# Kernel tuning notes

Measured on AMD Instinct MI355X. Metric: run time of the kernel, lower is better.

## Reference

```python
import jax, jax.numpy as jnp
import numpy as np

B, L, D, H, S = 16, 512, 512, 16, 3
FF = 4 * D
DH = D // H
EPS = 1e-5


def _bn(x, g, b):
    # BatchNorm1d in training mode: x is (B, C, L); biased variance over (B, L).
    m = jnp.mean(x, axis=(0, 2), keepdims=True)
    v = jnp.var(x, axis=(0, 2), keepdims=True)
    return (x - m) * jax.lax.rsqrt(v + EPS) * g[None, :, None] + b[None, :, None]


def setup_inputs() -> dict:
    key = jax.random.key(0)
    ks = jax.random.split(key, 8)
    s = 0.05
    return {
        "x": jax.random.normal(ks[0], (B, L, D), jnp.float32),
        "emb": jax.random.normal(ks[1], (D, D), jnp.float32) * s,  # emb[0], (in, out); hidden==input_dim
        "bn2_g": jnp.ones((D,), jnp.float32),
        "bn2_b": jnp.zeros((D,), jnp.float32),
        "Wq": jax.random.normal(ks[2], (S, D, D), jnp.float32) * s,  # stored (in,out)
        "bq": jnp.zeros((S, D), jnp.float32),
        "Wk": jax.random.normal(ks[3], (S, D, D), jnp.float32) * s,
        "bk": jnp.zeros((S, D), jnp.float32),
        "Wv": jax.random.normal(ks[4], (S, D, D), jnp.float32) * s,
        "bv": jnp.zeros((S, D), jnp.float32),
        "bna_g": jnp.ones((S, D), jnp.float32),
        "bna_b": jnp.zeros((S, D), jnp.float32),
        "W1": jax.random.normal(ks[5], (S, D, FF), jnp.float32) * s,  # conv1 1x1, (in,out)
        "b1": jnp.zeros((S, FF), jnp.float32),
        "W2": jax.random.normal(ks[6], (S, FF, D), jnp.float32) * s,  # conv2 1x1, (in,out)
        "b2": jnp.zeros((S, D), jnp.float32),
        "bnf_g": jnp.ones((S, D), jnp.float32),
        "bnf_b": jnp.zeros((S, D), jnp.float32),
    }


def _split_heads(t):
    # torch.cat(torch.split(t, D//H, dim=2), dim=0): (B,L,D) -> (H*B, L, DH), head-major on dim0.
    return jnp.moveaxis(t.reshape(B, L, H, DH), 2, 0).reshape(H * B, L, DH)


def reference(x, emb, bn2_g, bn2_b, Wq, bq, Wk, bk, Wv, bv, bna_g, bna_b,
              W1, b1, W2, b2, bnf_g, bnf_b):
    scale = 1.0 / np.sqrt(DH).astype(np.float32)
    xp = jnp.swapaxes(x, 1, 2)                      # (B, D, L)
    enc = jnp.einsum('bil,io->bol', xp, emb)        # 1x1 conv embedding, no bias
    enc = _bn(enc, bn2_g, bn2_b)                    # (B, D, L)
    for i in range(S):
        xin = jnp.swapaxes(enc, 1, 2)               # (B, L, D)
        Q = jax.nn.relu(xin @ Wq[i] + bq[i])
        K = jax.nn.relu(xin @ Wk[i] + bk[i])
        V = jax.nn.relu(xin @ Wv[i] + bv[i])
        Q_, K_, V_ = _split_heads(Q), _split_heads(K), _split_heads(V)  # (H*B, L, DH)
        sc = jnp.einsum('nqd,nkd->nqk', Q_, K_) * scale                 # (H*B, L, L)
        att = jax.nn.softmax(sc, axis=0)            # softmax over batch*heads dim (as in source)
        o = jnp.einsum('nqk,nkd->nqd', att, V_)     # (H*B, L, DH)
        # torch.cat(torch.split(o, B, dim=0), dim=2): (H*B,L,DH) -> (B,L,D)
        o = o.reshape(H, B, L, DH).transpose(1, 2, 0, 3).reshape(B, L, D)
        o = o + xin
        enc = _bn(jnp.swapaxes(o, 1, 2), bna_g[i], bna_b[i])            # (B, D, L)
        # FeedForward: 1x1 conv -> relu -> 1x1 conv -> residual -> BN
        h1 = jax.nn.relu(jnp.einsum('bdl,df->bfl', enc, W1[i]) + b1[i][None, :, None])
        h2 = jnp.einsum('bfl,fd->bdl', h1, W2[i]) + b2[i][None, :, None]
        enc = _bn(h2 + enc, bnf_g[i], bnf_b[i])
    return jnp.swapaxes(enc, 1, 2)                  # (B, L, D)
```

## Files before the change

### kernel.cpp

```cpp
#include <hip/hip_runtime.h>

#define DEVI __device__ __forceinline__

typedef unsigned short u16;
typedef __attribute__((ext_vector_type(8))) short s16x8;
typedef __attribute__((ext_vector_type(4))) float f32x4;
typedef __attribute__((ext_vector_type(4))) unsigned short u16x4v;
typedef __attribute__((ext_vector_type(2))) unsigned int u32x2;

constexpr int NB   = 16;
constexpr int LL   = 512;
constexpr int DD   = 512;
constexpr int FF_  = 2048;
constexpr int NROW = NB * LL;
constexpr float C2 = 0.17677669529663687f * 1.4426950408889634f;
constexpr size_t QKVOFF = (size_t)NROW * DD;

DEVI u16 f2b(float f) {
  unsigned int u = __float_as_uint(f);
  unsigned int r = u + 0x7FFFu + ((u >> 16) & 1u);
  return (u16)(r >> 16);
}

DEVI void gload16(const void* g, void* l) {
  __builtin_amdgcn_global_load_lds(
      (const __attribute__((address_space(1))) unsigned int*)(unsigned long long)g,
      (__attribute__((address_space(3))) unsigned int*)(unsigned int)(unsigned long long)l,
      16, 0, 0);
}

__global__ __launch_bounds__(256) void k_f32_to_bf16(const float* __restrict__ X, u16* __restrict__ Y, int n4) {
  for (int i = blockIdx.x * 256 + threadIdx.x; i < n4; i += gridDim.x * 256) {
    float4 x = ((const float4*)X)[i];
    u16x4v o; o[0] = f2b(x.x); o[1] = f2b(x.y); o[2] = f2b(x.z); o[3] = f2b(x.w);
    ((u16x4v*)Y)[i] = o;
  }
}

__global__ __launch_bounds__(256) void k_zero(float* __restrict__ p, int n) {
  int i = blockIdx.x * 256 + threadIdx.x;
  if (i < n) p[i] = 0.f;
}

__global__ __launch_bounds__(256) void k_recip(float* __restrict__ p, int n) {
  int i = blockIdx.x * 256 + threadIdx.x;
  if (i < n) p[i] = 1.0f / p[i];
}

__global__ void k_catbias(const float* __restrict__ a, const float* __restrict__ b,
                          const float* __restrict__ c, float* __restrict__ o) {
  int i = blockIdx.x * 256 + threadIdx.x;
  o[i] = (i < 512) ? a[i] : (i < 1024) ? b[i - 512] : c[i - 1024];
}

__global__ __launch_bounds__(256) void k_wtrans(const float* __restrict__ W, u16* __restrict__ WT, int K, int M) {
  __shared__ float tile[32][33];
  const int k0 = blockIdx.x * 32, m0 = blockIdx.y * 32;
  const int tx = threadIdx.x & 31, ty = threadIdx.x >> 5;
#pragma unroll
  for (int j = 0; j < 4; ++j) tile[ty + j * 8][tx] = W[(size_t)(k0 + ty + j * 8) * M + m0 + tx];
  __syncthreads();
#pragma unroll
  for (int j = 0; j < 4; ++j) WT[(size_t)(m0 + ty + j * 8) * K + k0 + tx] = f2b(tile[tx][ty + j * 8]);
}

template <int BM, int RELU, int HASB, int HASRES, int OUTF, int OUTB, int SPLIT3>
__global__ __launch_bounds__(256) void k_gemm(const u16* __restrict__ A, const u16* __restrict__ Bt,
                                              const float* __restrict__ bias, const float* __restrict__ Res,
                                              float* __restrict__ Cf, u16* __restrict__ Cb,
                                              int K, int Ncols) {
  constexpr int WR = BM / 64;
  constexpr int WC = 4 / WR;
  constexpr int MW = 4;
  constexpr int NW = 128 / (16 * WC);
  __shared__ __align__(16) u16 As[BM * 64];
  __shared__ __align__(16) u16 Bs[128 * 64];
  const int t = threadIdx.x, lane = t & 63, w = t >> 6;
  const int wr = w / WC, wc = w % WC, l16 = lane & 15, lhi = lane >> 4;
  const int row0 = blockIdx.x * BM, col0 = blockIdx.y * 128;
  const int sr = lane >> 3, sc = (lane & 7) * 8;
  const u16* Ag = A + (size_t)(row0 + sr) * K + sc;
  const u16* Bg = Bt + (size_t)(col0 + sr) * K + sc;

  f32x4 acc[MW][NW] = {};

  for (int k0 = 0; k0 < K; k0 += 64) {
    __syncthreads();
#pragma unroll
    for (int j = 0; j < BM / 32; ++j) {
      const int ch = w * (BM / 32) + j;
      gload16(Ag + (size_t)(ch * 8) * K + k0, As + ch * 512);
    }
#pragma unroll
    for (int j = 0; j < 4; ++j) {
      const int ch = w * 4 + j;
      gload16(Bg + (size_t)(ch * 8) * K + k0, Bs + ch * 512);
    }
    __syncthreads();
#pragma unroll
    for (int kk = 0; kk < 2; ++kk) {
      s16x8 af[MW], bfv[NW];
#pragma unroll
      for (int m = 0; m < MW; ++m) af[m] = *(const s16x8*)(As + (wr * 64 + m * 16 + l16) * 64 + kk * 32 + lhi * 8);
#pragma unroll
      for (int n = 0; n < NW; ++n) bfv[n] = *(const s16x8*)(Bs + (wc * (16 * NW) + n * 16 + l16) * 64 + kk * 32 + lhi * 8);
#pragma unroll
      for (int m = 0; m < MW; ++m)
#pragma unroll
        for (int n = 0; n < NW; ++n)
          acc[m][n] = __builtin_amdgcn_mfma_f32_16x16x32_bf16(af[m], bfv[n], acc[m][n], 0, 0, 0);
    }
  }

#pragma unroll
  for (int n = 0; n < NW; ++n) {
    const int col = col0 + wc * (16 * NW) + n * 16 + l16;
    float bv = 0.f;
    if constexpr (HASB) bv = bias[col];
#pragma unroll
    for (int m = 0; m < MW; ++m) {
      const int rbase = row0 + wr * 64 + m * 16 + lhi * 4;
#pragma unroll
      for (int r = 0; r < 4; ++r) {
        float v = acc[m][n][r] + bv;
        if constexpr (RELU) v = fmaxf(v, 0.f);
        const int row = rbase + r;
        const size_t idx = (size_t)row * Ncols + col;
        if constexpr (HASRES) v += Res[idx];
        if constexpr (OUTF) Cf[idx] = v;
        if constexpr (OUTB) {
          if constexpr (SPLIT3) {
            const size_t ib = (size_t)(col >> 9) * QKVOFF + (size_t)row * DD + (col & 511);
            Cb[ib] = f2b(v);
          } else {
            Cb[idx] = f2b(v);
          }
        }
      }
    }
  }
}

__global__ __launch_bounds__(256) void k_attn_z(const u16* __restrict__ Q, const u16* __restrict__ Kt,
                                                float* __restrict__ Z) {
  const int t = threadIdx.x, lane = t & 63, w = t >> 6;
  const int l16 = lane & 15, lhi = lane >> 4;
  const int q0 = blockIdx.x * 64 + (w >> 1) * 32;
  const int k0 = blockIdx.y * 64 + (w & 1) * 32;
  const int n0 = blockIdx.z * 16;
  f32x4 zac[2][2] = {};
  for (int nn = 0; nn < 16; ++nn) {
    const int n = n0 + nn, h = n >> 4, b = n & 15;
    const size_t base = (size_t)b * LL * DD + (size_t)h * 32;
    s16x8 a[2], bb[2];
#pragma unroll
    for (int mi = 0; mi < 2; ++mi) a[mi] = *(const s16x8*)(Q + base + (size_t)(q0 + mi * 16 + l16) * DD + lhi * 8);
#pragma unroll
    for (int ni = 0; ni < 2; ++ni) bb[ni] = *(const s16x8*)(Kt + base + (size_t)(k0 + ni * 16 + l16) * DD + lhi * 8);
#pragma unroll
    for (int mi = 0; mi < 2; ++mi)
#pragma unroll
      for (int ni = 0; ni < 2; ++ni) {
        f32x4 z4 = {0.f, 0.f, 0.f, 0.f};
        f32x4 s = __builtin_amdgcn_mfma_f32_16x16x32_bf16(a[mi], bb[ni], z4, 0, 0, 0);
#pragma unroll
        for (int r = 0; r < 4; ++r) zac[mi][ni][r] += exp2f(s[r] * C2);
      }
  }
#pragma unroll
  for (int mi = 0; mi < 2; ++mi)
#pragma unroll
    for (int ni = 0; ni < 2; ++ni)
#pragma unroll
      for (int r = 0; r < 4; ++r)
        atomicAdd(&Z[(q0 + mi * 16 + lhi * 4 + r) * LL + k0 + ni * 16 + l16], zac[mi][ni][r]);
}

__global__ __launch_bounds__(512) void k_attn_pv3(const u16* __restrict__ Q, const u16* __restrict__ K,
                                                  const u16* __restrict__ V, const float* __restrict__ IZ,
                                                  const float* __restrict__ Res, float* __restrict__ T) {
  __shared__ __align__(16) u16 Kl[512 * 40];
  __shared__ __align__(16) u16 Vl[32 * 520];
  __shared__ __align__(16) u16 Pl[8][1024];
  const int n = blockIdx.x, h = n >> 4, b = n & 15;
  const int t = threadIdx.x, lane = t & 63, w = t >> 6;
  const int l16 = lane & 15, lhi = lane >> 4;
  const size_t base = (size_t)b * LL * DD + (size_t)h * 32;

#pragma unroll
  for (int j = 0; j < 4; ++j) {
    const int c = t + j * 512;
    const int k = c >> 2, part = c & 3;
    const s16x8 v = *(const s16x8*)(K + base + (size_t)k * DD + part * 8);
    *(s16x8*)(Kl + k * 40 + part * 8) = v;
  }
#pragma unroll
  for (int j = 0; j < 4; ++j) {
    const int c = t + j * 512;
    const int k = c >> 2, dp = c & 3;
    const s16x8 v = *(const s16x8*)(V + base + (size_t)k * DD + dp * 8);
#pragma unroll
    for (int jj = 0; jj < 8; ++jj) Vl[(dp * 8 + jj) * 520 + k] = (u16)v[jj];
  }
  const int qbase = w * 64;
  s16x8 aqv[4];
#pragma unroll
  for (int qf = 0; qf < 4; ++qf)
    aqv[qf] = *(const s16x8*)(Q + base + (size_t)(qbase + qf * 16 + l16) * DD + lhi * 8);
  __syncthreads();

  char* P = (char*)&Pl[w][0];
  const int wxor = (l16 & 7) << 4;
  const int wbase = l16 * 128 + lhi * 8;

#pragma unroll
  for (int qf = 0; qf < 4; ++qf) {
    const int q16 = qbase + qf * 16;
    const float* izrow = IZ + (size_t)(q16 + l16) * LL + lhi * 4;
    f32x4 oa[2] = {};
#pragma unroll
    for (int kt = 0; kt < 8; ++kt) {
      const int kb = kt * 64;
      f32x4 s[4]; float4 iz[4];
#pragma unroll
      for (int ks = 0; ks < 4; ++ks) {
        const s16x8 af = *(const s16x8*)(Kl + (kb + ks * 16 + l16) * 40 + lhi * 8);
        f32x4 z4 = {0.f, 0.f, 0.f, 0.f};
        s[ks] = __builtin_amdgcn_mfma_f32_16x16x32_bf16(af, aqv[qf], z4, 0, 0, 0);
        iz[ks] = *(const float4*)(izrow + kb + ks * 16);
      }
#pragma unroll
      for (int ks = 0; ks < 4; ++ks) {
        const float p0 = exp2f(s[ks][0] * C2) * iz[ks].x;
        const float p1 = exp2f(s[ks][1] * C2) * iz[ks].y;
        const float p2 = exp2f(s[ks][2] * C2) * iz[ks].z;
        const float p3 = exp2f(s[ks][3] * C2) * iz[ks].w;
        unsigned int pk0, pk1;
        asm("v_cvt_pk_bf16_f32 %0, %1, %2" : "=v"(pk0) : "v"(p0), "v"(p1));
        asm("v_cvt_pk_bf16_f32 %0, %1, %2" : "=v"(pk1) : "v"(p2), "v"(p3));
        u32x2 pw; pw[0] = pk0; pw[1] = pk1;
        *(u32x2*)(P + ((wbase + ks * 32) ^ wxor)) = pw;
      }
#pragma unroll
      for (int kc = 0; kc < 2; ++kc) {
        const s16x8 pa = *(const s16x8*)(P + ((l16 * 128 + kc * 64 + lhi * 16) ^ wxor));
#pragma unroll
        for (int dt = 0; dt < 2; ++dt) {
          const s16x8 bv = *(const s16x8*)(Vl + (dt * 16 + l16) * 520 + kb + kc * 32 + lhi * 8);
          oa[dt] = __builtin_amdgcn_mfma_f32_16x16x32_bf16(pa, bv, oa[dt], 0, 0, 0);
        }
      }
    }
#pragma unroll
    for (int dt = 0; dt < 2; ++dt)
#pragma unroll
      for (int r = 0; r < 4; ++r) {
        const size_t idx = (size_t)(b * LL + q16 + lhi * 4 + r) * DD + h * 32 + dt * 16 + l16;
        T[idx] = oa[dt][r] + Res[idx];
      }
  }
}

__global__ __launch_bounds__(256) void k_bn_stats(const float* __restrict__ X, float* __restrict__ S) {
  const int t = threadIdx.x;
  const int r0 = blockIdx.x * 32;
  float s0 = 0.f, q0 = 0.f, s1 = 0.f, q1 = 0.f;
  for (int r = 0; r < 32; ++r) {
    const float x0 = X[(size_t)(r0 + r) * DD + t];
    const float x1 = X[(size_t)(r0 + r) * DD + t + 256];
    s0 += x0; q0 += x0 * x0; s1 += x1; q1 += x1 * x1;
  }
  atomicAdd(&S[t], s0);
  atomicAdd(&S[t + 256], s1);
  atomicAdd(&S[512 + t], q0);
  atomicAdd(&S[512 + t + 256], q1);
}

__global__ void k_bn_fin(float* __restrict__ S, const float* __restrict__ g,
                         const float* __restrict__ be, float* __restrict__ coef) {
  const int d = threadIdx.x;
  const float inv = 1.0f / 8192.0f;
  const float mean = S[d] * inv;
  const float var = S[512 + d] * inv - mean * mean;
  const float a = rsqrtf(var + 1e-5f) * g[d];
  coef[d] = a;
  coef[512 + d] = be[d] - mean * a;
  S[d] = 0.f; S[512 + d] = 0.f;
}

template <int WB>
__global__ __launch_bounds__(256) void k_bn_apply(const float* __restrict__ X, const float* __restrict__ coef,
                                                  float* __restrict__ Yf, u16* __restrict__ Yb) {
  const int n4 = NROW * DD / 4;
  for (int i = blockIdx.x * 256 + threadIdx.x; i < n4; i += gridDim.x * 256) {
    const float4 xv = ((const float4*)X)[i];
    const int d = (i & 127) * 4;
    const float y0 = fmaf(xv.x, coef[d + 0], coef[512 + d + 0]);
    const float y1 = fmaf(xv.y, coef[d + 1], coef[512 + d + 1]);
    const float y2 = fmaf(xv.z, coef[d + 2], coef[512 + d + 2]);
    const float y3 = fmaf(xv.w, coef[d + 3], coef[512 + d + 3]);
    ((float4*)Yf)[i] = make_float4(y0, y1, y2, y3);
    if constexpr (WB) {
      u16x4v o; o[0] = f2b(y0); o[1] = f2b(y1); o[2] = f2b(y2); o[3] = f2b(y3);
      ((u16x4v*)Yb)[i] = o;
    }
  }
}

extern "C" void kernel_launch(void* const* d_in, const int* in_sizes, int n_in,
                              void* d_out, int out_size, void* d_ws, size_t ws_size,
                              hipStream_t stream) {
  const float* x    = (const float*)d_in[0];
  const float* emb  = (const float*)d_in[1];
  const float* bn2g = (const float*)d_in[2];
  const float* bn2b = (const float*)d_in[3];
  const float* Wq   = (const float*)d_in[4];
  const float* bq   = (const float*)d_in[5];
  const float* Wk   = (const float*)d_in[6];
  const float* bkp  = (const float*)d_in[7];
  const float* Wv   = (const float*)d_in[8];
  const float* bvp  = (const float*)d_in[9];
  const float* bnag = (const float*)d_in[10];
  const float* bnab = (const float*)d_in[11];
  const float* W1   = (const float*)d_in[12];
  const float* b1   = (const float*)d_in[13];
  const float* W2   = (const float*)d_in[14];
  const float* b2   = (const float*)d_in[15];
  const float* bnfg = (const float*)d_in[16];
  const float* bnfb = (const float*)d_in[17];

  char* p = (char*)d_ws;
  auto alloc = [&](size_t bytes) { char* r = p; p += (bytes + 255) & ~(size_t)255; return r; };
  u16*   xb    = (u16*)alloc((size_t)NROW * DD * 2);
  float* encF  = (float*)alloc((size_t)NROW * DD * 4);
  u16*   encB  = (u16*)alloc((size_t)NROW * DD * 2);
  float* tF    = (float*)alloc((size_t)NROW * DD * 4);
  u16*   qkv   = (u16*)alloc((size_t)3 * NROW * DD * 2);
  u16*   h1    = (u16*)alloc((size_t)NROW * FF_ * 2);
  float* Z     = (float*)alloc((size_t)LL * LL * 4);
  float* sums  = (float*)alloc(1024 * 4);
  float* coef  = (float*)alloc(1024 * 4);
  float* bqkv  = (float*)alloc(1536 * 4);
  u16*   embT  = (u16*)alloc((size_t)DD * DD * 2);
  u16*   wqkvT = (u16*)alloc((size_t)3 * DD * DD * 2);
  u16*   w1T   = (u16*)alloc((size_t)DD * FF_ * 2);
  u16*   w2T   = (u16*)alloc((size_t)FF_ * DD * 2);
  if ((size_t)(p - (char*)d_ws) > ws_size) return;

  auto run_bn = [&](const float* Xs, const float* g, const float* be, float* Yf, u16* Yb) {
    k_bn_stats<<<256, 256, 0, stream>>>(Xs, sums);
    k_bn_fin<<<1, 512, 0, stream>>>(sums, g, be, coef);
    if (Yb) k_bn_apply<1><<<2048, 256, 0, stream>>>(Xs, coef, Yf, Yb);
    else    k_bn_apply<0><<<2048, 256, 0, stream>>>(Xs, coef, Yf, nullptr);
  };

  k_zero<<<4, 256, 0, stream>>>(sums, 1024);
  k_f32_to_bf16<<<2048, 256, 0, stream>>>(x, xb, NROW * DD / 4);
  k_wtrans<<<dim3(16, 16), 256, 0, stream>>>(emb, embT, DD, DD);
  k_gemm<64, 0, 0, 0, 1, 0, 0><<<dim3(128, 4), 256, 0, stream>>>(xb, embT, nullptr, nullptr, tF, nullptr, DD, DD);
  run_bn(tF, bn2g, bn2b, encF, encB);

  for (int i = 0; i < 3; ++i) {
    k_wtrans<<<dim3(16, 16), 256, 0, stream>>>(Wq + (size_t)i * DD * DD, wqkvT, DD, DD);
    k_wtrans<<<dim3(16, 16), 256, 0, stream>>>(Wk + (size_t)i * DD * DD, wqkvT + (size_t)512 * DD, DD, DD);
    k_wtrans<<<dim3(16, 16), 256, 0, stream>>>(Wv + (size_t)i * DD * DD, wqkvT + (size_t)1024 * DD, DD, DD);
    k_catbias<<<6, 256, 0, stream>>>(bq + i * DD, bkp + i * DD, bvp + i * DD, bqkv);
    k_gemm<128, 1, 1, 0, 0, 1, 1><<<dim3(64, 12), 256, 0, stream>>>(encB, wqkvT, bqkv, nullptr, nullptr, qkv, DD, 1536);
    k_zero<<<1024, 256, 0, stream>>>(Z, LL * LL);
    k_attn_z<<<dim3(8, 8, 16), 256, 0, stream>>>(qkv, qkv + QKVOFF, Z);
    k_recip<<<1024, 256, 0, stream>>>(Z, LL * LL);
    k_attn_pv3<<<256, 512, 0, stream>>>(qkv, qkv + QKVOFF, qkv + 2 * QKVOFF, Z, encF, tF);
    run_bn(tF, bnag + i * DD, bnab + i * DD, encF, encB);
    k_wtrans<<<dim3(16, 64), 256, 0, stream>>>(W1 + (size_t)i * DD * FF_, w1T, DD, FF_);
    k_gemm<128, 1, 1, 0, 0, 1, 0><<<dim3(64, 16), 256, 0, stream>>>(encB, w1T, b1 + i * FF_, nullptr, nullptr, h1, DD, FF_);
    k_wtrans<<<dim3(64, 16), 256, 0, stream>>>(W2 + (size_t)i * FF_ * DD, w2T, FF_, DD);
    k_gemm<64, 0, 1, 1, 1, 0, 0><<<dim3(128, 4), 256, 0, stream>>>(h1, w2T, b2 + i * DD, encF, tF, nullptr, FF_, DD);
    float* yf = (i == 2) ? (float*)d_out : encF;
    run_bn(tF, bnfg + i * DD, bnfb + i * DD, yf, (i == 2) ? nullptr : encB);
  }
}
```

Baseline: 728.6 us.

## Fuse BatchNorm statistics into GEMM and attention epilogues

```diff
diff --git a/kernel.cpp b/kernel.cpp
--- a/kernel.cpp
+++ b/kernel.cpp
@@ -64,11 +64,11 @@
   for (int j = 0; j < 4; ++j) WT[(size_t)(m0 + ty + j * 8) * K + k0 + tx] = f2b(tile[tx][ty + j * 8]);
 }
 
-template <int BM, int RELU, int HASB, int HASRES, int OUTF, int OUTB, int SPLIT3>
+template <int BM, int RELU, int HASB, int HASRES, int OUTF, int OUTB, int STATS, int SPLIT3>
 __global__ __launch_bounds__(256) void k_gemm(const u16* __restrict__ A, const u16* __restrict__ Bt,
                                               const float* __restrict__ bias, const float* __restrict__ Res,
                                               float* __restrict__ Cf, u16* __restrict__ Cb,
-                                              int K, int Ncols) {
+                                              float* __restrict__ stats, int K, int Ncols) {
   constexpr int WR = BM / 64;
   constexpr int WC = 4 / WR;
   constexpr int MW = 4;
@@ -117,6 +117,7 @@
     const int col = col0 + wc * (16 * NW) + n * 16 + l16;
     float bv = 0.f;
     if constexpr (HASB) bv = bias[col];
+    float ssum = 0.f, ssq = 0.f;
 #pragma unroll
     for (int m = 0; m < MW; ++m) {
       const int rbase = row0 + wr * 64 + m * 16 + lhi * 4;
@@ -136,6 +137,15 @@
             Cb[idx] = f2b(v);
           }
         }
+        if constexpr (STATS) { ssum += v; ssq += v * v; }
+      }
+    }
+    if constexpr (STATS) {
+      ssum += __shfl_xor(ssum, 16); ssq += __shfl_xor(ssq, 16);
+      ssum += __shfl_xor(ssum, 32); ssq += __shfl_xor(ssq, 32);
+      if (lhi == 0) {
+        atomicAdd(&stats[col], ssum);
+        atomicAdd(&stats[512 + col], ssq);
       }
     }
   }
@@ -178,7 +188,8 @@
 
 __global__ __launch_bounds__(512) void k_attn_pv3(const u16* __restrict__ Q, const u16* __restrict__ K,
                                                   const u16* __restrict__ V, const float* __restrict__ IZ,
-                                                  const float* __restrict__ Res, float* __restrict__ T) {
+                                                  const float* __restrict__ Res, float* __restrict__ T,
+                                                  float* __restrict__ stats) {
   __shared__ __align__(16) u16 Kl[512 * 40];
   __shared__ __align__(16) u16 Vl[32 * 520];
   __shared__ __align__(16) u16 Pl[8][1024];
@@ -212,6 +223,7 @@
   char* P = (char*)&Pl[w][0];
   const int wxor = (l16 & 7) << 4;
   const int wbase = l16 * 128 + lhi * 8;
+  float ssum[2] = {0.f, 0.f}, ssq[2] = {0.f, 0.f};
 
 #pragma unroll
   for (int qf = 0; qf < 4; ++qf) {
@@ -256,24 +268,22 @@
 #pragma unroll
       for (int r = 0; r < 4; ++r) {
         const size_t idx = (size_t)(b * LL + q16 + lhi * 4 + r) * DD + h * 32 + dt * 16 + l16;
-        T[idx] = oa[dt][r] + Res[idx];
-      }
-  }
-}
-
-__global__ __launch_bounds__(256) void k_bn_stats(const float* __restrict__ X, float* __restrict__ S) {
-  const int t = threadIdx.x;
-  const int r0 = blockIdx.x * 32;
-  float s0 = 0.f, q0 = 0.f, s1 = 0.f, q1 = 0.f;
-  for (int r = 0; r < 32; ++r) {
-    const float x0 = X[(size_t)(r0 + r) * DD + t];
-    const float x1 = X[(size_t)(r0 + r) * DD + t + 256];
-    s0 += x0; q0 += x0 * x0; s1 += x1; q1 += x1 * x1;
-  }
-  atomicAdd(&S[t], s0);
-  atomicAdd(&S[t + 256], s1);
-  atomicAdd(&S[512 + t], q0);
-  atomicAdd(&S[512 + t + 256], q1);
+        const float v = oa[dt][r] + Res[idx];
+        T[idx] = v;
+        ssum[dt] += v; ssq[dt] += v * v;
+      }
+  }
+#pragma unroll
+  for (int dt = 0; dt < 2; ++dt) {
+    float su = ssum[dt], sq = ssq[dt];
+    su += __shfl_xor(su, 16); sq += __shfl_xor(sq, 16);
+    su += __shfl_xor(su, 32); sq += __shfl_xor(sq, 32);
+    if (lhi == 0) {
+      const int col = h * 32 + dt * 16 + l16;
+      atomicAdd(&stats[col], su);
+      atomicAdd(&stats[512 + col], sq);
+    }
+  }
 }
 
 __global__ void k_bn_fin(float* __restrict__ S, const float* __restrict__ g,
@@ -348,7 +358,6 @@
   if ((size_t)(p - (char*)d_ws) > ws_size) return;
 
   auto run_bn = [&](const float* Xs, const float* g, const float* be, float* Yf, u16* Yb) {
-    k_bn_stats<<<256, 256, 0, stream>>>(Xs, sums);
     k_bn_fin<<<1, 512, 0, stream>>>(sums, g, be, coef);
     if (Yb) k_bn_apply<1><<<2048, 256, 0, stream>>>(Xs, coef, Yf, Yb);
     else    k_bn_apply<0><<<2048, 256, 0, stream>>>(Xs, coef, Yf, nullptr);
@@ -357,7 +366,7 @@
   k_zero<<<4, 256, 0, stream>>>(sums, 1024);
   k_f32_to_bf16<<<2048, 256, 0, stream>>>(x, xb, NROW * DD / 4);
   k_wtrans<<<dim3(16, 16), 256, 0, stream>>>(emb, embT, DD, DD);
-  k_gemm<64, 0, 0, 0, 1, 0, 0><<<dim3(128, 4), 256, 0, stream>>>(xb, embT, nullptr, nullptr, tF, nullptr, DD, DD);
+  k_gemm<128, 0, 0, 0, 1, 0, 1, 0><<<dim3(64, 4), 256, 0, stream>>>(xb, embT, nullptr, nullptr, tF, nullptr, sums, DD, DD);
   run_bn(tF, bn2g, bn2b, encF, encB);
 
   for (int i = 0; i < 3; ++i) {
@@ -365,16 +374,16 @@
     k_wtrans<<<dim3(16, 16), 256, 0, stream>>>(Wk + (size_t)i * DD * DD, wqkvT + (size_t)512 * DD, DD, DD);
     k_wtrans<<<dim3(16, 16), 256, 0, stream>>>(Wv + (size_t)i * DD * DD, wqkvT + (size_t)1024 * DD, DD, DD);
     k_catbias<<<6, 256, 0, stream>>>(bq + i * DD, bkp + i * DD, bvp + i * DD, bqkv);
-    k_gemm<128, 1, 1, 0, 0, 1, 1><<<dim3(64, 12), 256, 0, stream>>>(encB, wqkvT, bqkv, nullptr, nullptr, qkv, DD, 1536);
+    k_gemm<128, 1, 1, 0, 0, 1, 0, 1><<<dim3(64, 12), 256, 0, stream>>>(encB, wqkvT, bqkv, nullptr, nullptr, qkv, nullptr, DD, 1536);
     k_zero<<<1024, 256, 0, stream>>>(Z, LL * LL);
     k_attn_z<<<dim3(8, 8, 16), 256, 0, stream>>>(qkv, qkv + QKVOFF, Z);
     k_recip<<<1024, 256, 0, stream>>>(Z, LL * LL);
-    k_attn_pv3<<<256, 512, 0, stream>>>(qkv, qkv + QKVOFF, qkv + 2 * QKVOFF, Z, encF, tF);
+    k_attn_pv3<<<256, 512, 0, stream>>>(qkv, qkv + QKVOFF, qkv + 2 * QKVOFF, Z, encF, tF, sums);
     run_bn(tF, bnag + i * DD, bnab + i * DD, encF, encB);
     k_wtrans<<<dim3(16, 64), 256, 0, stream>>>(W1 + (size_t)i * DD * FF_, w1T, DD, FF_);
-    k_gemm<128, 1, 1, 0, 0, 1, 0><<<dim3(64, 16), 256, 0, stream>>>(encB, w1T, b1 + i * FF_, nullptr, nullptr, h1, DD, FF_);
+    k_gemm<128, 1, 1, 0, 0, 1, 0, 0><<<dim3(64, 16), 256, 0, stream>>>(encB, w1T, b1 + i * FF_, nullptr, nullptr, h1, nullptr, DD, FF_);
     k_wtrans<<<dim3(64, 16), 256, 0, stream>>>(W2 + (size_t)i * FF_ * DD, w2T, FF_, DD);
-    k_gemm<64, 0, 1, 1, 1, 0, 0><<<dim3(128, 4), 256, 0, stream>>>(h1, w2T, b2 + i * DD, encF, tF, nullptr, FF_, DD);
+    k_gemm<128, 0, 1, 1, 1, 0, 1, 0><<<dim3(64, 4), 256, 0, stream>>>(h1, w2T, b2 + i * DD, encF, tF, nullptr, sums, FF_, DD);
     float* yf = (i == 2) ? (float*)d_out : encF;
     run_bn(tF, bnfg + i * DD, bnfb + i * DD, yf, (i == 2) ? nullptr : encB);
   }
```

Measured after the change: 717.4 us. No clear change (-1.5%).
